# Performance work log

Hardware: AMD Instinct MI355X
Metric: run time of the kernel (lower is better)

The kernel has to match this reference:

```python
import jax, jax.numpy as jnp
import numpy as np

B, C = 2, 2
D = H = W = 192
N_BIF = 64                 # bif ids 0..63; labels = bif*4 + stub (stub in 1..3)
NUM_LABELS = 4 * N_BIF     # 256
MIN_STUBS = 2
MIN_VOXELS = 1
TEMP = 0.2


def setup_inputs() -> dict:
    key = jax.random.key(0)
    k1, k2 = jax.random.split(key)
    pred = jax.random.normal(k1, (B, C, D, H, W), dtype=jnp.float32)
    stub_label_map = jax.random.randint(k2, (B, 1, D, H, W), 0, NUM_LABELS).astype(jnp.float32)
    return {"pred": pred, "stub_label_map": stub_label_map}


def reference(pred, stub_label_map):
    # foreground probability: softmax over channel dim, take class 1
    fg = jax.nn.softmax(pred, axis=1)[:, 1]                     # [B,D,H,W]
    labels = jnp.round(stub_label_map[:, 0]).astype(jnp.int32)  # [B,D,H,W]

    Bn = fg.shape[0]
    fg_flat = fg.reshape(Bn, -1)
    lab_flat = labels.reshape(Bn, -1)

    seg = lambda v, i: jax.ops.segment_sum(v, i, num_segments=NUM_LABELS)
    sums = jax.vmap(seg)(fg_flat, lab_flat)                      # [B, NUM_LABELS]
    counts = jax.vmap(seg)(jnp.ones_like(fg_flat), lab_flat)     # [B, NUM_LABELS]

    # group labels as [bif, stub]; drop bif 0 and stub 0 (never used in loop)
    sums = sums.reshape(Bn, N_BIF, 4)[:, 1:, 1:4]                # [B, N_BIF-1, 3]
    counts = counts.reshape(Bn, N_BIF, 4)[:, 1:, 1:4]

    valid = counts >= MIN_VOXELS                                 # stub has enough voxels
    means = sums / jnp.maximum(counts, 1.0)                      # per-stub mean fg prob

    # softmin over the valid stubs of each bif (masked softmax of -mean/temp)
    logits = jnp.where(valid, -means / TEMP, -1e9)
    weights = jax.nn.softmax(logits, axis=-1)
    score = jnp.sum(jnp.where(valid, means * weights, 0.0), axis=-1)  # [B, N_BIF-1]

    valid_bif = jnp.sum(valid, axis=-1) >= MIN_STUBS
    total = jnp.sum(jnp.where(valid_bif, 1.0 - score, 0.0))
    n_bifs = jnp.sum(valid_bif)
    return jnp.where(n_bifs > 0, total / jnp.maximum(n_bifs, 1).astype(total.dtype), 0.0)
```

## Files before the change

kernel.cpp:

```cpp
#include <hip/hip_runtime.h>
#include <math.h>

#define BATCH     2
#define NLAB      256
#define VOX       (192*192*192)
#define TEMP      0.2f
#define GRIDX     768
#define NITER     ((VOX/4)/(GRIDX*256))
#define NPART     16

#define STEP      4096.0f
#define INV_STEP  (1.0f/4096.0f)

typedef unsigned int u32;
typedef __attribute__((ext_vector_type(8))) short bf16x8;
typedef __attribute__((ext_vector_type(4))) float f32x4;
union FragU { uint4 u; bf16x8 v; };

__device__ __forceinline__ void voxprep(float pa, float pc, float pl,
                                        u32& fg16, u32& w0) {
    const float fg = __builtin_amdgcn_rcpf(1.0f + __expf(pa - pc));
    u32 bits = __float_as_uint(fg);
    bits += 0x7FFFu + ((bits >> 16) & 1u);
    fg16 = bits >> 16;
    const u32 lab = ((u32)(int)(pl + 0.5f)) & 255u;
    w0 = (1u << (lab >> 4)) + ((1u << (lab & 15u)) << 16);
}

#define PAIR2(w0e, w0o, fp, aw, b1w, b2w) do {                              \
    const u32 _he = ((w0e) >> mlane) & 1u;                                  \
    const u32 _ho = ((w0o) >> mlane) & 1u;                                  \
    const u32 _le = ((w0e) >> m16) & 1u;                                    \
    const u32 _lo = ((w0o) >> m16) & 1u;                                    \
    const u32 _hpk = _he + (_ho << 16);                                     \
    const u32 _lpk = _le + (_lo << 16);                                     \
    aw  = __umul24(_hpk, 0x3F80u);                                          \
    b1w = __umul24(_lpk, 0x3F80u);                                          \
    b2w = (fp) & __umul24(_lpk, 0xFFFFu);                                   \
} while (0)

__global__ __launch_bounds__(256) void histo_kernel(
    const float* __restrict__ pred,
    const float* __restrict__ labmap,
    float* __restrict__ ws_slots)
{
    __shared__ __align__(16) u32 s_w0[4][2][256];
    __shared__ __align__(16) u32 s_fg[4][2][128];

    const int b    = blockIdx.y;
    const int tid  = threadIdx.x;
    const int w    = tid >> 6;
    const int lane = tid & 63;
    const u32 mlane = (u32)(lane & 15);
    const u32 m16   = mlane + 16u;
    const int g    = lane >> 4;

    const float4* p0 = (const float4*)(pred + (size_t)b * 2 * VOX);
    const float4* p1 = (const float4*)(pred + (size_t)b * 2 * VOX + VOX);
    const float4* lm = (const float4*)(labmap + (size_t)b * VOX);

    f32x4 accC = {0.f, 0.f, 0.f, 0.f};
    f32x4 accS = {0.f, 0.f, 0.f, 0.f};

    const int base = blockIdx.x * 256 + tid;

    #pragma unroll 2
    for (int it = 0; it < NITER; ++it) {
        const int i = base + it * (GRIDX * 256);
        const float4 a = p0[i];
        const float4 c = p1[i];
        const float4 l = lm[i];

        u32 f0, f1, f2, f3, w00, w01, w02, w03;
        voxprep(a.x, c.x, l.x, f0, w00);
        voxprep(a.y, c.y, l.y, f1, w01);
        voxprep(a.z, c.z, l.z, f2, w02);
        voxprep(a.w, c.w, l.w, f3, w03);

        u32* stw = &s_w0[w][it & 1][0];
        u32* stf = &s_fg[w][it & 1][0];
        *(uint4*)(stw + (lane << 2)) = make_uint4(w00, w01, w02, w03);
        *(uint2*)(stf + (lane << 1)) = make_uint2(f0 + (f1 << 16),
                                                  f2 + (f3 << 16));

        const u32* rp = stw + (g << 3);
        const u32* rf = stf + (g << 2);
        #pragma unroll
        for (int t = 0; t < 8; ++t) {
            const uint4 q0 = *(const uint4*)(rp + t * 32);
            const uint4 q1 = *(const uint4*)(rp + t * 32 + 4);
            const uint4 fq = *(const uint4*)(rf + t * 16);
            u32 a0, a1, a2, a3, b10, b11, b12, b13, b20, b21, b22, b23;
            PAIR2(q0.x, q0.y, fq.x, a0, b10, b20);
            PAIR2(q0.z, q0.w, fq.y, a1, b11, b21);
            PAIR2(q1.x, q1.y, fq.z, a2, b12, b22);
            PAIR2(q1.z, q1.w, fq.w, a3, b13, b23);
            FragU A, B1, B2;
            A.u  = make_uint4(a0, a1, a2, a3);
            B1.u = make_uint4(b10, b11, b12, b13);
            B2.u = make_uint4(b20, b21, b22, b23);
            accC = __builtin_amdgcn_mfma_f32_16x16x32_bf16(A.v, B1.v, accC, 0, 0, 0);
            accS = __builtin_amdgcn_mfma_f32_16x16x32_bf16(A.v, B2.v, accS, 0, 0, 0);
        }
    }

    float* cnt_w = (float*)&s_w0[w][0][0];
    float* sum_w = (float*)&s_w0[w][1][0];
    const int row0 = (lane >> 4) << 2;
    const int colb = lane & 15;
    #pragma unroll
    for (int j = 0; j < 4; ++j) {
        cnt_w[(row0 + j) * 16 + colb] = accC[j];
        sum_w[(row0 + j) * 16 + colb] = accS[j];
    }
    __syncthreads();

    float cs = 0.0f, ss = 0.0f;
    #pragma unroll
    for (int ww = 0; ww < 4; ++ww) {
        cs += ((float*)&s_w0[ww][0][0])[tid];
        ss += ((float*)&s_w0[ww][1][0])[tid];
    }
    ws_slots[((size_t)(b * GRIDX + blockIdx.x)) * NLAB + tid] = ss + STEP * cs;
}

__global__ __launch_bounds__(256) void reduce_kernel(
    const float* __restrict__ ws_slots,
    float* __restrict__ psum,
    float* __restrict__ pcnt)
{
    const int bin  = threadIdx.x;
    const int b    = blockIdx.x / NPART;
    const int part = blockIdx.x % NPART;
    const int per  = GRIDX / NPART;

    float cs = 0.0f, ss = 0.0f;
    for (int s = part * per; s < (part + 1) * per; ++s) {
        float v = ws_slots[((size_t)(b * GRIDX + s)) * NLAB + bin];
        float c = floorf(v * INV_STEP + 0.5f);
        cs += c;
        ss += v - c * STEP;
    }
    psum[(size_t)blockIdx.x * NLAB + bin] = ss;
    pcnt[(size_t)blockIdx.x * NLAB + bin] = cs;
}

__global__ __launch_bounds__(256) void scalar_kernel(
    const float* __restrict__ psum,
    const float* __restrict__ pcnt,
    float* __restrict__ out)
{
    __shared__ float s_fsum[BATCH][NLAB];
    __shared__ float s_fcnt[BATCH][NLAB];

    const int tid = threadIdx.x;

    for (int b = 0; b < BATCH; ++b) {
        float ss = 0.0f, cs = 0.0f;
        for (int p = 0; p < NPART; ++p) {
            ss += psum[(size_t)(b * NPART + p) * NLAB + tid];
            cs += pcnt[(size_t)(b * NPART + p) * NLAB + tid];
        }
        s_fsum[b][tid] = ss;
        s_fcnt[b][tid] = cs;
    }
    __syncthreads();

    if (tid < 64) {
        float total = 0.0f;
        float nbifs = 0.0f;
        if (tid >= 1) {
            for (int bb = 0; bb < BATCH; ++bb) {
                float means[3];
                bool  valid[3];
                int   nvalid = 0;
                for (int s = 0; s < 3; ++s) {
                    int lab = tid * 4 + 1 + s;
                    float cnt = s_fcnt[bb][lab];
                    float sum = s_fsum[bb][lab];
                    valid[s] = (cnt >= 1.0f);
                    means[s] = sum / fmaxf(cnt, 1.0f);
                    nvalid  += valid[s] ? 1 : 0;
                }
                float logits[3], m = -3e38f;
                for (int s = 0; s < 3; ++s) {
                    logits[s] = valid[s] ? (-means[s] / TEMP) : -1e9f;
                    m = fmaxf(m, logits[s]);
                }
                float e[3], se = 0.0f;
                for (int s = 0; s < 3; ++s) { e[s] = __expf(logits[s] - m); se += e[s]; }
                float score = 0.0f;
                for (int s = 0; s < 3; ++s) {
                    if (valid[s]) score += means[s] * (e[s] / se);
                }
                if (nvalid >= 2) {
                    total += 1.0f - score;
                    nbifs += 1.0f;
                }
            }
        }
        for (int off = 32; off > 0; off >>= 1) {
            total += __shfl_down(total, off);
            nbifs += __shfl_down(nbifs, off);
        }
        if (tid == 0) {
            out[0] = (nbifs > 0.0f) ? (total / fmaxf(nbifs, 1.0f)) : 0.0f;
        }
    }
}

extern "C" void kernel_launch(void* const* d_in, const int* in_sizes, int n_in,
                              void* d_out, int out_size, void* d_ws, size_t ws_size,
                              hipStream_t stream) {
    const float* pred = (const float*)d_in[0];
    const float* lab  = (const float*)d_in[1];

    float* ws_slots = (float*)d_ws;
    float* psum = ws_slots + (size_t)BATCH * GRIDX * NLAB;
    float* pcnt = psum + (size_t)BATCH * NPART * NLAB;

    dim3 grid(GRIDX, BATCH);
    histo_kernel<<<grid, 256, 0, stream>>>(pred, lab, ws_slots);
    reduce_kernel<<<BATCH * NPART, 256, 0, stream>>>(ws_slots, psum, pcnt);
    scalar_kernel<<<1, 256, 0, stream>>>(psum, pcnt, (float*)d_out);
}
```

Before: 210.9 us.

## Prefetch next iteration loads and pre-pack one-hot masks to cut bit ops

Adds software pipelining to the histogram loop. The next iteration's pred and label float4 loads are issued before the current voxels are processed, replacing the previous unroll-by-2. The one-hot hi/lo masks are also packed pairwise in the producer lanes, so each consumer extracts both bf16 halves with a single shift and a 0x10001 mask instead of four shifts plus packing. This trims ALU work in the inner MFMA feed loop at the cost of extra registers for the prefetched data, plus a redundant reload on the last iteration.

```diff
diff --git a/kernel.cpp b/kernel.cpp
--- a/kernel.cpp
+++ b/kernel.cpp
@@ -17,26 +17,25 @@
 typedef __attribute__((ext_vector_type(4))) float f32x4;
 union FragU { uint4 u; bf16x8 v; };
 
-__device__ __forceinline__ void voxprep(float pa, float pc, float pl,
-                                        u32& fg16, u32& w0) {
+__device__ __forceinline__ u32 fgbf16(float pa, float pc) {
     const float fg = __builtin_amdgcn_rcpf(1.0f + __expf(pa - pc));
     u32 bits = __float_as_uint(fg);
     bits += 0x7FFFu + ((bits >> 16) & 1u);
-    fg16 = bits >> 16;
+    return bits >> 16;
+}
+
+__device__ __forceinline__ void voxmask(float pl, u32& hm, u32& lmm) {
     const u32 lab = ((u32)(int)(pl + 0.5f)) & 255u;
-    w0 = (1u << (lab >> 4)) + ((1u << (lab & 15u)) << 16);
-}
-
-#define PAIR2(w0e, w0o, fp, aw, b1w, b2w) do {                              \
-    const u32 _he = ((w0e) >> mlane) & 1u;                                  \
-    const u32 _ho = ((w0o) >> mlane) & 1u;                                  \
-    const u32 _le = ((w0e) >> m16) & 1u;                                    \
-    const u32 _lo = ((w0o) >> m16) & 1u;                                    \
-    const u32 _hpk = _he + (_ho << 16);                                     \
-    const u32 _lpk = _le + (_lo << 16);                                     \
-    aw  = __umul24(_hpk, 0x3F80u);                                          \
-    b1w = __umul24(_lpk, 0x3F80u);                                          \
-    b2w = (fp) & __umul24(_lpk, 0xFFFFu);                                   \
+    hm  = 1u << (lab >> 4);
+    lmm = 1u << (lab & 15u);
+}
+
+#define PAIRH(whi, wlo, fp, aw, b1w, b2w) do {                              \
+    const u32 _h = ((whi) >> mlane) & 0x10001u;                             \
+    const u32 _l = ((wlo) >> mlane) & 0x10001u;                             \
+    aw  = __umul24(_h, 0x3F80u);                                            \
+    b1w = __umul24(_l, 0x3F80u);                                            \
+    b2w = (fp) & __umul24(_l, 0xFFFFu);                                     \
 } while (0)
 
 __global__ __launch_bounds__(256) void histo_kernel(
@@ -44,7 +43,7 @@
     const float* __restrict__ labmap,
     float* __restrict__ ws_slots)
 {
-    __shared__ __align__(16) u32 s_w0[4][2][256];
+    __shared__ __align__(16) u32 s_iv[4][2][256];
     __shared__ __align__(16) u32 s_fg[4][2][128];
 
     const int b    = blockIdx.y;
@@ -52,7 +51,6 @@
     const int w    = tid >> 6;
     const int lane = tid & 63;
     const u32 mlane = (u32)(lane & 15);
-    const u32 m16   = mlane + 16u;
     const int g    = lane >> 4;
 
     const float4* p0 = (const float4*)(pred + (size_t)b * 2 * VOX);
@@ -64,37 +62,46 @@
 
     const int base = blockIdx.x * 256 + tid;
 
-    #pragma unroll 2
+    float4 a = p0[base];
+    float4 c = p1[base];
+    float4 l = lm[base];
+
     for (int it = 0; it < NITER; ++it) {
-        const int i = base + it * (GRIDX * 256);
-        const float4 a = p0[i];
-        const float4 c = p1[i];
-        const float4 l = lm[i];
-
-        u32 f0, f1, f2, f3, w00, w01, w02, w03;
-        voxprep(a.x, c.x, l.x, f0, w00);
-        voxprep(a.y, c.y, l.y, f1, w01);
-        voxprep(a.z, c.z, l.z, f2, w02);
-        voxprep(a.w, c.w, l.w, f3, w03);
-
-        u32* stw = &s_w0[w][it & 1][0];
-        u32* stf = &s_fg[w][it & 1][0];
-        *(uint4*)(stw + (lane << 2)) = make_uint4(w00, w01, w02, w03);
-        *(uint2*)(stf + (lane << 1)) = make_uint2(f0 + (f1 << 16),
-                                                  f2 + (f3 << 16));
-
-        const u32* rp = stw + (g << 3);
-        const u32* rf = stf + (g << 2);
+        const int nit = (it + 1 < NITER) ? (it + 1) : it;
+        const int inx = base + nit * (GRIDX * 256);
+        const float4 an = p0[inx];
+        const float4 cn = p1[inx];
+        const float4 ln = lm[inx];
+
+        u32 hm0, lm0, hm1, lm1, hm2, lm2, hm3, lm3;
+        voxmask(l.x, hm0, lm0);
+        voxmask(l.y, hm1, lm1);
+        voxmask(l.z, hm2, lm2);
+        voxmask(l.w, hm3, lm3);
+        const u32 whiA = hm0 | (hm1 << 16);
+        const u32 wloA = lm0 | (lm1 << 16);
+        const u32 whiB = hm2 | (hm3 << 16);
+        const u32 wloB = lm2 | (lm3 << 16);
+        const u32 fgA  = fgbf16(a.x, c.x) | (fgbf16(a.y, c.y) << 16);
+        const u32 fgB  = fgbf16(a.z, c.z) | (fgbf16(a.w, c.w) << 16);
+
+        u32* iv  = &s_iv[w][it & 1][0];
+        u32* fgp = &s_fg[w][it & 1][0];
+        *(uint4*)(iv + (lane << 2)) = make_uint4(whiA, wloA, whiB, wloB);
+        *(uint2*)(fgp + (lane << 1)) = make_uint2(fgA, fgB);
+
+        const u32* rp = iv + (g << 3);
+        const u32* rf = fgp + (g << 2);
         #pragma unroll
         for (int t = 0; t < 8; ++t) {
             const uint4 q0 = *(const uint4*)(rp + t * 32);
             const uint4 q1 = *(const uint4*)(rp + t * 32 + 4);
             const uint4 fq = *(const uint4*)(rf + t * 16);
             u32 a0, a1, a2, a3, b10, b11, b12, b13, b20, b21, b22, b23;
-            PAIR2(q0.x, q0.y, fq.x, a0, b10, b20);
-            PAIR2(q0.z, q0.w, fq.y, a1, b11, b21);
-            PAIR2(q1.x, q1.y, fq.z, a2, b12, b22);
-            PAIR2(q1.z, q1.w, fq.w, a3, b13, b23);
+            PAIRH(q0.x, q0.y, fq.x, a0, b10, b20);
+            PAIRH(q0.z, q0.w, fq.y, a1, b11, b21);
+            PAIRH(q1.x, q1.y, fq.z, a2, b12, b22);
+            PAIRH(q1.z, q1.w, fq.w, a3, b13, b23);
             FragU A, B1, B2;
             A.u  = make_uint4(a0, a1, a2, a3);
             B1.u = make_uint4(b10, b11, b12, b13);
@@ -102,10 +109,12 @@
             accC = __builtin_amdgcn_mfma_f32_16x16x32_bf16(A.v, B1.v, accC, 0, 0, 0);
             accS = __builtin_amdgcn_mfma_f32_16x16x32_bf16(A.v, B2.v, accS, 0, 0, 0);
         }
-    }
-
-    float* cnt_w = (float*)&s_w0[w][0][0];
-    float* sum_w = (float*)&s_w0[w][1][0];
+
+        a = an; c = cn; l = ln;
+    }
+
+    float* cnt_w = (float*)&s_iv[w][0][0];
+    float* sum_w = (float*)&s_iv[w][1][0];
     const int row0 = (lane >> 4) << 2;
     const int colb = lane & 15;
     #pragma unroll
@@ -118,8 +127,8 @@
     float cs = 0.0f, ss = 0.0f;
     #pragma unroll
     for (int ww = 0; ww < 4; ++ww) {
-        cs += ((float*)&s_w0[ww][0][0])[tid];
-        ss += ((float*)&s_w0[ww][1][0])[tid];
+        cs += ((float*)&s_iv[ww][0][0])[tid];
+        ss += ((float*)&s_iv[ww][1][0])[tid];
     }
     ws_slots[((size_t)(b * GRIDX + blockIdx.x)) * NLAB + tid] = ss + STEP * cs;
 }
```

Measured after the change: 209.1 us. About the same (-0.9%).
